# Optimization experiments

Hardware: AMD Instinct MI355X
Metric: run time of the kernel (lower is better)

## Reference

```python
import jax, jax.numpy as jnp
import numpy as np

N = 50000      # num nodes
E = 600000     # num edges
D = 128        # num_node_features (in == out)
R = 8          # num_relations


def setup_inputs() -> dict:
    key = jax.random.key(0)
    k = jax.random.split(key, 6)
    x = jax.random.normal(k[0], (N, D), dtype=jnp.float32)
    edge_index = jax.random.randint(k[1], (2, E), 0, N, dtype=jnp.int32)
    edge_type = jax.random.randint(k[2], (E,), 0, R, dtype=jnp.int32)
    scale = 1.0 / np.sqrt(D).astype(np.float32)
    weight = jax.random.normal(k[3], (R, D, D), dtype=jnp.float32) * scale  # per-relation W_r
    root = jax.random.normal(k[4], (D, D), dtype=jnp.float32) * scale       # self-loop weight
    bias = jnp.zeros((D,), dtype=jnp.float32)
    return {"x": x, "edge_index": edge_index, "edge_type": edge_type,
            "weight": weight, "root": root, "bias": bias}


def _rgcn(x, weight, root, bias, edge_index, edge_type):
    # RGCNConv (PyG defaults: aggr='mean' per relation, root weight + bias)
    src, dst = edge_index[0], edge_index[1]
    # combined segment id over (relation, dst) so one segment_sum covers all relations
    seg = edge_type * N + dst                              # [E]
    msgs = x[src]                                          # [E, D] gather
    sums = jax.ops.segment_sum(msgs, seg, num_segments=R * N)                 # [R*N, D]
    cnts = jax.ops.segment_sum(jnp.ones((E, 1), x.dtype), seg, num_segments=R * N)
    mean = sums / jnp.maximum(cnts, 1.0)                   # mean over neighbors, 0 if none
    agg = mean.reshape(R, N, D)
    out = jnp.einsum('rnd,rde->ne', agg, weight) + x @ root + bias
    return out


def reference(x, edge_index, edge_type, weight, root, bias):
    return jax.nn.relu(_rgcn(x, weight, root, bias, edge_index, edge_type))
```

## Files before the change

### kernel.cpp

```cpp
#include <hip/hip_runtime.h>

constexpr int NN = 50000;
constexpr int NE = 600000;
constexpr int D  = 128;
constexpr int NR = 8;
constexpr int KT = (NR + 1) * D;
constexpr int NSEG = NN * NR;

constexpr int SCAN_ELEMS = 1024;
constexpr int NBLK2 = (NSEG + SCAN_ELEMS - 1) / SCAN_ELEMS;

typedef unsigned int   u32;
typedef unsigned short u16;
typedef float  f32x4 __attribute__((ext_vector_type(4)));
typedef short  s16x8 __attribute__((ext_vector_type(8)));

__device__ __forceinline__ u16 f2bf(float f) {
    u32 u = __float_as_uint(f);
    u32 r = (u + 0x7fffu + ((u >> 16) & 1u)) >> 16;
    return (u16)r;
}

__device__ __forceinline__ void async_cp16(const void* g, void* l) {
    __builtin_amdgcn_global_load_lds(
        (const __attribute__((address_space(1))) u32*)g,
        (__attribute__((address_space(3))) u32*)l, 16, 0, 0);
}

__global__ __launch_bounds__(256) void prep_all(const float* __restrict__ x,
                                                const float* __restrict__ weight,
                                                const float* __restrict__ root,
                                                const int* __restrict__ dst,
                                                const int* __restrict__ et,
                                                u16* __restrict__ xb,
                                                u16* __restrict__ wt,
                                                u16* __restrict__ rt,
                                                int* __restrict__ cnt2) {
    const int NX4 = NN * D / 4;
    const int NW  = (NR + 1) * D * D;
    int gid = blockIdx.x * 256 + threadIdx.x;
    if (gid < NX4) {
        int i = gid * 4;
        float4 v = *(const float4*)(x + i);
        ushort4 o;
        o.x = f2bf(v.x); o.y = f2bf(v.y); o.z = f2bf(v.z); o.w = f2bf(v.w);
        *(ushort4*)(xb + i) = o;
        return;
    }
    int g = gid - NX4;
    if (g < NW) {
        int p = g >> 14;
        int idx = g & 16383;
        int n = idx >> 7, k = idx & 127;
        float v = (p < NR) ? weight[(size_t)p * D * D + k * D + n] : root[k * D + n];
        u16* dp = (p < NR) ? (wt + (size_t)p * D * D) : rt;
        dp[idx] = f2bf(v);
        return;
    }
    int e = g - NW;
    if (e < NE) atomicAdd(&cnt2[dst[e] * NR + et[e]], 1);
}

__global__ __launch_bounds__(256) void scan1(const int* __restrict__ cnt,
                                             int* __restrict__ offs,
                                             int* __restrict__ bsums) {
    __shared__ int lds[256];
    int t = threadIdx.x;
    int base = blockIdx.x * SCAN_ELEMS + t * 4;
    int v0 = (base + 0 < NSEG) ? cnt[base + 0] : 0;
    int v1 = (base + 1 < NSEG) ? cnt[base + 1] : 0;
    int v2 = (base + 2 < NSEG) ? cnt[base + 2] : 0;
    int v3 = (base + 3 < NSEG) ? cnt[base + 3] : 0;
    int s = v0 + v1 + v2 + v3;
    lds[t] = s;
    __syncthreads();
    int val = s;
    for (int off = 1; off < 256; off <<= 1) {
        int tmp = (t >= off) ? lds[t - off] : 0;
        __syncthreads();
        val += tmp;
        lds[t] = val;
        __syncthreads();
    }
    int ex = val - s;
    if (base + 0 < NSEG) offs[base + 0] = ex;
    if (base + 1 < NSEG) offs[base + 1] = ex + v0;
    if (base + 2 < NSEG) offs[base + 2] = ex + v0 + v1;
    if (base + 3 < NSEG) offs[base + 3] = ex + v0 + v1 + v2;
    if (t == 255) bsums[blockIdx.x] = val;
}

__global__ __launch_bounds__(512) void scan2(int* __restrict__ bsums) {
    __shared__ int lds[512];
    int t = threadIdx.x;
    int v = (t < NBLK2) ? bsums[t] : 0;
    lds[t] = v;
    __syncthreads();
    int val = v;
    for (int off = 1; off < 512; off <<= 1) {
        int tmp = (t >= off) ? lds[t - off] : 0;
        __syncthreads();
        val += tmp;
        lds[t] = val;
        __syncthreads();
    }
    if (t < NBLK2) bsums[t] = val - v;
}

__global__ __launch_bounds__(256) void scan3(int* __restrict__ offs,
                                             int* __restrict__ cur,
                                             const int* __restrict__ bsums) {
    int i = blockIdx.x * 256 + threadIdx.x;
    if (i < NSEG) {
        int v = offs[i] + bsums[i >> 10];
        offs[i] = v;
        cur[i]  = v;
    }
    if (i == 0) offs[NSEG] = NE;
}

__global__ __launch_bounds__(256) void fill_bins(const int* __restrict__ src,
                                                 const int* __restrict__ dst,
                                                 const int* __restrict__ et,
                                                 int* __restrict__ cur,
                                                 int* __restrict__ ebin) {
    int e = blockIdx.x * 256 + threadIdx.x;
    if (e >= NE) return;
    int r = et[e];
    int idx = atomicAdd(&cur[dst[e] * NR + r], 1);
    ebin[idx] = (r << 16) | src[e];
}

__global__ __launch_bounds__(128) void aggregate_kernel(const u32* __restrict__ xw,
                                                        const int* __restrict__ offs2,
                                                        const int* __restrict__ ebin,
                                                        u32* __restrict__ sw) {
    const int lane = threadIdx.x & 63;
    const int n = blockIdx.x * 2 + (threadIdx.x >> 6);
    if (n >= NN) return;
    const int beg = __builtin_amdgcn_readfirstlane(offs2[n * NR]);
    const int c   = __builtin_amdgcn_readfirstlane(offs2[n * NR + NR]) - beg;

    float a0 = 0.f, a1 = 0.f;
    int r_cur = 0, cnt_cur = 0;

    int q0 = 0, q1 = 0, q2 = 0, q3 = 0, q4 = 0, q5 = 0, q6 = 0, q7 = 0;
    u32 v0 = 0, v1 = 0, v2 = 0, v3 = 0, v4 = 0, v5 = 0, v6 = 0, v7 = 0;

#define REFILL(Q, V, IDX)                                                   \
    if ((IDX) < c) {                                                        \
        Q = __builtin_amdgcn_readfirstlane(ebin[beg + (IDX)]);              \
        V = xw[(size_t)((u32)Q & 0xffffu) * 64 + lane];                     \
    }
#define FLUSH()                                                             \
    {                                                                       \
        float inv_ = 1.0f / (float)(cnt_cur > 0 ? cnt_cur : 1);             \
        u32 lo16_ = f2bf(a0 * inv_);                                        \
        u32 hi16_ = f2bf(a1 * inv_);                                        \
        sw[((size_t)r_cur * NN + n) * 64 + lane] = lo16_ | (hi16_ << 16);   \
        a0 = 0.f; a1 = 0.f; cnt_cur = 0; ++r_cur;                           \
    }
#define CONSUME(Q, V)                                                       \
    {                                                                       \
        int rj_ = (int)((u32)(Q) >> 16);                                    \
        while (r_cur < rj_) FLUSH()                                         \
        a0 += __uint_as_float((V) << 16);                                   \
        a1 += __uint_as_float((V) & 0xffff0000u);                           \
        ++cnt_cur;                                                          \
    }

    REFILL(q0, v0, 0) REFILL(q1, v1, 1) REFILL(q2, v2, 2) REFILL(q3, v3, 3)
    REFILL(q4, v4, 4) REFILL(q5, v5, 5) REFILL(q6, v6, 6) REFILL(q7, v7, 7)

    int e = 0;
    for (; e + 8 <= c; e += 8) {
        CONSUME(q0, v0) REFILL(q0, v0, e + 8)
        CONSUME(q1, v1) REFILL(q1, v1, e + 9)
        CONSUME(q2, v2) REFILL(q2, v2, e + 10)
        CONSUME(q3, v3) REFILL(q3, v3, e + 11)
        CONSUME(q4, v4) REFILL(q4, v4, e + 12)
        CONSUME(q5, v5) REFILL(q5, v5, e + 13)
        CONSUME(q6, v6) REFILL(q6, v6, e + 14)
        CONSUME(q7, v7) REFILL(q7, v7, e + 15)
    }
    if (e + 0 < c) CONSUME(q0, v0)
    if (e + 1 < c) CONSUME(q1, v1)
    if (e + 2 < c) CONSUME(q2, v2)
    if (e + 3 < c) CONSUME(q3, v3)
    if (e + 4 < c) CONSUME(q4, v4)
    if (e + 5 < c) CONSUME(q5, v5)
    if (e + 6 < c) CONSUME(q6, v6)
    if (e + 7 < c) CONSUME(q7, v7)

    while (r_cur < NR) FLUSH()
#undef REFILL
#undef FLUSH
#undef CONSUME
}

__global__ __launch_bounds__(256) void mfma_gemm(const u16* __restrict__ xb,
                                                 const u16* __restrict__ sums,
                                                 const u16* __restrict__ rt,
                                                 const u16* __restrict__ wt,
                                                 const float* __restrict__ bias,
                                                 float* __restrict__ out) {
    __shared__ u16 As[64 * 32];
    __shared__ u16 Bs[128 * 32];

    const int tid  = threadIdx.x;
    const int wave = tid >> 6;
    const int lane = tid & 63;
    const int m0   = blockIdx.x * 64;

    f32x4 acc[8];
#pragma unroll
    for (int j = 0; j < 8; ++j) acc[j] = (f32x4){0.f, 0.f, 0.f, 0.f};

    const int srow = 16 * wave + (lane >> 2);
    const int sch  = (lane & 3) * 8;

    for (int k0 = 0; k0 < KT; k0 += 32) {
        const int rpl = k0 >> 7;
        const int kof = k0 & 127;
        const u16* Ap = (rpl == 0) ? xb : sums + (size_t)(rpl - 1) * NN * D;
        const u16* Bp = (rpl == 0) ? rt : wt + (size_t)(rpl - 1) * D * D;

        __syncthreads();
        {
            int ga = m0 + srow; if (ga > NN - 1) ga = NN - 1;
            async_cp16(Ap + (size_t)ga * D + kof + sch, (char*)As + wave * 1024);
            async_cp16(Bp + (size_t)srow * D + kof + sch, (char*)Bs + wave * 1024);
            async_cp16(Bp + (size_t)(64 + srow) * D + kof + sch,
                       (char*)Bs + 4096 + wave * 1024);
        }
        __syncthreads();

        const int fr = lane & 15;
        const int fk = (lane >> 4) * 8;
        s16x8 af = *(const s16x8*)&As[(16 * wave + fr) * 32 + fk];
#pragma unroll
        for (int nt = 0; nt < 8; ++nt) {
            s16x8 bf = *(const s16x8*)&Bs[(nt * 16 + fr) * 32 + fk];
            acc[nt] = __builtin_amdgcn_mfma_f32_16x16x32_bf16(af, bf, acc[nt], 0, 0, 0);
        }
    }

    const int cl = lane & 15;
    const int rq = (lane >> 4) * 4;
#pragma unroll
    for (int nt = 0; nt < 8; ++nt) {
        int col = nt * 16 + cl;
        float bv = bias[col];
#pragma unroll
        for (int reg = 0; reg < 4; ++reg) {
            int n = m0 + 16 * wave + rq + reg;
            if (n < NN) {
                float v = acc[nt][reg] + bv;
                out[(size_t)n * D + col] = fmaxf(v, 0.0f);
            }
        }
    }
}

extern "C" void kernel_launch(void* const* d_in, const int* in_sizes, int n_in,
                              void* d_out, int out_size, void* d_ws, size_t ws_size,
                              hipStream_t stream) {
    const float* x      = (const float*)d_in[0];
    const int*   ei     = (const int*)d_in[1];
    const int*   et     = (const int*)d_in[2];
    const float* weight = (const float*)d_in[3];
    const float* root   = (const float*)d_in[4];
    const float* bias   = (const float*)d_in[5];
    float* out = (float*)d_out;
    const int* srcv = ei;
    const int* dstv = ei + NE;

    int* cnt2  = (int*)d_ws;
    int* cur2  = cnt2 + NSEG;
    int* offs2 = cur2 + NSEG;
    int* bsums = offs2 + NSEG + 1;
    int* ebin  = bsums + 512;
    size_t fixed_b  = ((char*)(ebin + NE) - (char*)d_ws);
    size_t fixed_al = (fixed_b + 255) & ~(size_t)255;
    u16* xb   = (u16*)((char*)d_ws + fixed_al);
    u16* sums = xb + (size_t)NN * D;
    u16* wt   = sums + (size_t)NR * NN * D;
    u16* rt   = wt + (size_t)NR * D * D;

    hipMemsetAsync(cnt2, 0, NSEG * sizeof(int), stream);

    const int PREP = NN * D / 4 + (NR + 1) * D * D + NE;
    prep_all<<<(PREP + 255) / 256, 256, 0, stream>>>(x, weight, root, dstv, et,
                                                     xb, wt, rt, cnt2);

    scan1<<<NBLK2, 256, 0, stream>>>(cnt2, offs2, bsums);
    scan2<<<1, 512, 0, stream>>>(bsums);
    scan3<<<(NSEG + 256) / 256, 256, 0, stream>>>(offs2, cur2, bsums);
    fill_bins<<<(NE + 255) / 256, 256, 0, stream>>>(srcv, dstv, et, cur2, ebin);

    aggregate_kernel<<<(NN + 1) / 2, 128, 0, stream>>>((const u32*)xb, offs2, ebin,
                                                       (u32*)sums);

    mfma_gemm<<<(NN + 63) / 64, 256, 0, stream>>>(xb, sums, rt, wt, bias, out);
}
```

Baseline: 221.6 us.

## Restructure GEMM with per-wave double-buffered B staging and direct A register loads

```diff
diff --git a/kernel.cpp b/kernel.cpp
--- a/kernel.cpp
+++ b/kernel.cpp
@@ -33,8 +33,7 @@
                                                 const int* __restrict__ dst,
                                                 const int* __restrict__ et,
                                                 u16* __restrict__ xb,
-                                                u16* __restrict__ wt,
-                                                u16* __restrict__ rt,
+                                                u16* __restrict__ wt9,
                                                 int* __restrict__ cnt2) {
     const int NX4 = NN * D / 4;
     const int NW  = (NR + 1) * D * D;
@@ -52,9 +51,9 @@
         int p = g >> 14;
         int idx = g & 16383;
         int n = idx >> 7, k = idx & 127;
-        float v = (p < NR) ? weight[(size_t)p * D * D + k * D + n] : root[k * D + n];
-        u16* dp = (p < NR) ? (wt + (size_t)p * D * D) : rt;
-        dp[idx] = f2bf(v);
+        float v = (p == 0) ? root[k * D + n]
+                           : weight[(size_t)(p - 1) * D * D + k * D + n];
+        wt9[(size_t)p * 16384 + idx] = f2bf(v);
         return;
     }
     int e = g - NW;
@@ -200,49 +199,86 @@
 
 __global__ __launch_bounds__(256) void mfma_gemm(const u16* __restrict__ xb,
                                                  const u16* __restrict__ sums,
-                                                 const u16* __restrict__ rt,
-                                                 const u16* __restrict__ wt,
+                                                 const u16* __restrict__ wt9,
                                                  const float* __restrict__ bias,
                                                  float* __restrict__ out) {
-    __shared__ u16 As[64 * 32];
-    __shared__ u16 Bs[128 * 32];
+    __shared__ __align__(16) u16 Bs[4][2][128 * 32];
 
     const int tid  = threadIdx.x;
     const int wave = tid >> 6;
     const int lane = tid & 63;
-    const int m0   = blockIdx.x * 64;
-
-    f32x4 acc[8];
-#pragma unroll
-    for (int j = 0; j < 8; ++j) acc[j] = (f32x4){0.f, 0.f, 0.f, 0.f};
-
-    const int srow = 16 * wave + (lane >> 2);
-    const int sch  = (lane & 3) * 8;
-
-    for (int k0 = 0; k0 < KT; k0 += 32) {
-        const int rpl = k0 >> 7;
-        const int kof = k0 & 127;
-        const u16* Ap = (rpl == 0) ? xb : sums + (size_t)(rpl - 1) * NN * D;
-        const u16* Bp = (rpl == 0) ? rt : wt + (size_t)(rpl - 1) * D * D;
-
-        __syncthreads();
-        {
-            int ga = m0 + srow; if (ga > NN - 1) ga = NN - 1;
-            async_cp16(Ap + (size_t)ga * D + kof + sch, (char*)As + wave * 1024);
-            async_cp16(Bp + (size_t)srow * D + kof + sch, (char*)Bs + wave * 1024);
-            async_cp16(Bp + (size_t)(64 + srow) * D + kof + sch,
-                       (char*)Bs + 4096 + wave * 1024);
+    const int m0   = blockIdx.x * 128;
+    const int fr   = lane & 15;
+    const int fk   = (lane >> 4) * 8;
+
+    int boff[8];
+#pragma unroll
+    for (int r = 0; r < 8; ++r) {
+        int p = r * 64 + lane;
+        int g = p ^ ((p >> 3) & 7);
+        boff[r] = (g >> 2) * D + (g & 3) * 8;
+    }
+    int bidx[8];
+#pragma unroll
+    for (int nt = 0; nt < 8; ++nt) {
+        int gl = (nt * 16 + fr) * 4 + (lane >> 4);
+        int pp = gl ^ ((gl >> 3) & 7);
+        bidx[nt] = pp * 8;
+    }
+
+    int r0 = m0 + wave * 32 + fr;        if (r0 > NN - 1) r0 = NN - 1;
+    int r1 = m0 + wave * 32 + 16 + fr;   if (r1 > NN - 1) r1 = NN - 1;
+    const size_t aoff0 = (size_t)r0 * D + fk;
+    const size_t aoff1 = (size_t)r1 * D + fk;
+
+    u16* myB0 = &Bs[wave][0][0];
+    u16* myB1 = &Bs[wave][1][0];
+
+    auto stage = [&](u16* bufp, const u16* Bp) {
+#pragma unroll
+        for (int r = 0; r < 8; ++r)
+            async_cp16(Bp + boff[r], (char*)bufp + (r * 64 + lane) * 16);
+    };
+
+    f32x4 acc[2][8];
+#pragma unroll
+    for (int i = 0; i < 2; ++i)
+#pragma unroll
+        for (int j = 0; j < 8; ++j) acc[i][j] = (f32x4){0.f, 0.f, 0.f, 0.f};
+
+    stage(myB0, wt9);
+    __builtin_amdgcn_sched_barrier(0);
+    s16x8 a0c = *(const s16x8*)(xb + aoff0);
+    s16x8 a1c = *(const s16x8*)(xb + aoff1);
+
+    for (int it = 0; it < KT / 32 - 1; ++it) {
+        const int nx  = it + 1;
+        const int rpl = nx >> 2;
+        const int kof = (nx & 3) * 32;
+        u16* nbuf = (nx & 1) ? myB1 : myB0;
+        const u16* cbuf = (it & 1) ? myB1 : myB0;
+
+        stage(nbuf, wt9 + rpl * (D * D) + kof);
+        __builtin_amdgcn_sched_barrier(0);
+        const u16* Ap = ((rpl == 0) ? xb : sums + (size_t)(rpl - 1) * NN * D) + kof;
+        s16x8 a0n = *(const s16x8*)(Ap + aoff0);
+        s16x8 a1n = *(const s16x8*)(Ap + aoff1);
+        __builtin_amdgcn_sched_barrier(0);
+        asm volatile("s_waitcnt vmcnt(10)" ::: "memory");
+#pragma unroll
+        for (int nt = 0; nt < 8; ++nt) {
+            s16x8 bf = *(const s16x8*)(cbuf + bidx[nt]);
+            acc[0][nt] = __builtin_amdgcn_mfma_f32_16x16x32_bf16(a0c, bf, acc[0][nt], 0, 0, 0);
+            acc[1][nt] = __builtin_amdgcn_mfma_f32_16x16x32_bf16(a1c, bf, acc[1][nt], 0, 0, 0);
         }
-        __syncthreads();
-
-        const int fr = lane & 15;
-        const int fk = (lane >> 4) * 8;
-        s16x8 af = *(const s16x8*)&As[(16 * wave + fr) * 32 + fk];
-#pragma unroll
-        for (int nt = 0; nt < 8; ++nt) {
-            s16x8 bf = *(const s16x8*)&Bs[(nt * 16 + fr) * 32 + fk];
-            acc[nt] = __builtin_amdgcn_mfma_f32_16x16x32_bf16(af, bf, acc[nt], 0, 0, 0);
-        }
+        a0c = a0n; a1c = a1n;
+    }
+    asm volatile("s_waitcnt vmcnt(0)" ::: "memory");
+#pragma unroll
+    for (int nt = 0; nt < 8; ++nt) {
+        s16x8 bf = *(const s16x8*)(myB1 + bidx[nt]);
+        acc[0][nt] = __builtin_amdgcn_mfma_f32_16x16x32_bf16(a0c, bf, acc[0][nt], 0, 0, 0);
+        acc[1][nt] = __builtin_amdgcn_mfma_f32_16x16x32_bf16(a1c, bf, acc[1][nt], 0, 0, 0);
     }
 
     const int cl = lane & 15;
@@ -252,13 +288,15 @@
         int col = nt * 16 + cl;
         float bv = bias[col];
 #pragma unroll
-        for (int reg = 0; reg < 4; ++reg) {
-            int n = m0 + 16 * wave + rq + reg;
-            if (n < NN) {
-                float v = acc[nt][reg] + bv;
-                out[(size_t)n * D + col] = fmaxf(v, 0.0f);
+        for (int rg = 0; rg < 2; ++rg)
+#pragma unroll
+            for (int reg = 0; reg < 4; ++reg) {
+                int n = m0 + wave * 32 + rg * 16 + rq + reg;
+                if (n < NN) {
+                    float v = acc[rg][nt][reg] + bv;
+                    out[(size_t)n * D + col] = fmaxf(v, 0.0f);
+                }
             }
-        }
     }
 }
 
@@ -284,14 +322,13 @@
     size_t fixed_al = (fixed_b + 255) & ~(size_t)255;
     u16* xb   = (u16*)((char*)d_ws + fixed_al);
     u16* sums = xb + (size_t)NN * D;
-    u16* wt   = sums + (size_t)NR * NN * D;
-    u16* rt   = wt + (size_t)NR * D * D;
+    u16* wt9  = sums + (size_t)NR * NN * D;
 
     hipMemsetAsync(cnt2, 0, NSEG * sizeof(int), stream);
 
     const int PREP = NN * D / 4 + (NR + 1) * D * D + NE;
     prep_all<<<(PREP + 255) / 256, 256, 0, stream>>>(x, weight, root, dstv, et,
-                                                     xb, wt, rt, cnt2);
+                                                     xb, wt9, cnt2);
 
     scan1<<<NBLK2, 256, 0, stream>>>(cnt2, offs2, bsums);
     scan2<<<1, 512, 0, stream>>>(bsums);
@@ -301,5 +338,5 @@
     aggregate_kernel<<<(NN + 1) / 2, 128, 0, stream>>>((const u32*)xb, offs2, ebin,
                                                        (u32*)sums);
 
-    mfma_gemm<<<(NN + 63) / 64, 256, 0, stream>>>(xb, sums, rt, wt, bias, out);
-}
+    mfma_gemm<<<(NN + 127) / 128, 256, 0, stream>>>(xb, sums, wt9, bias, out);
+}
```

Result: slower. 237.2 us (+7.1%).
